# Optimization experiments

Hardware: AMD Instinct MI355X
Metric: run time of the kernel (lower is better)

## Reference

```python
import jax, jax.numpy as jnp
import numpy as np

N_NODES = 50000
N_EDGES = 200000
D = 384
R = 2  # num_relations


def setup_inputs() -> dict:
    key = jax.random.key(0)
    ks = jax.random.split(key, 16)
    inp = {
        "embeddings": jax.random.normal(ks[0], (N_NODES, D), dtype=jnp.float32),
        "edge_index": jax.random.randint(ks[1], (2, N_EDGES), 0, N_NODES, dtype=jnp.int64),
        "edge_type": jax.random.randint(ks[2], (N_EDGES,), 0, R, dtype=jnp.int64),
    }
    # RGCNConv params for 3 layers: per-relation weight, root weight, bias
    s = 1.0 / np.sqrt(D)
    for i, kk in zip((1, 2, 3), range(3)):
        inp[f"W{i}"] = jax.random.uniform(ks[3 + 3 * kk], (R, D, D), dtype=jnp.float32, minval=-s, maxval=s)
        inp[f"root{i}"] = jax.random.uniform(ks[4 + 3 * kk], (D, D), dtype=jnp.float32, minval=-s, maxval=s)
        inp[f"bias{i}"] = jnp.zeros((D,), dtype=jnp.float32)
    return inp


def _rgcn_conv(x, src, dst, edge_type, W, root, bias):
    # PyG RGCNConv with aggr='mean': for each relation, mean-aggregate neighbor
    # features over edges of that relation, then apply relation weight; plus
    # root transform and bias. We transform-then-aggregate (equivalent, linear).
    out = x @ root + bias
    for r in range(R):
        xr = x @ W[r]                                   # [N, D]
        mask = (edge_type == r).astype(x.dtype)         # [E]
        msg = xr[src] * mask[:, None]                   # [E, D] gather
        s = jax.ops.segment_sum(msg, dst, num_segments=N_NODES)    # [N, D]
        cnt = jax.ops.segment_sum(mask, dst, num_segments=N_NODES)  # [N]
        out = out + s / jnp.maximum(cnt, 1.0)[:, None]  # mean (0 if no edges)
    return out


def reference(embeddings, edge_index, edge_type, W1, root1, bias1, W2, root2, bias2, W3, root3, bias3):
    src, dst = edge_index[0], edge_index[1]
    x = jax.nn.relu(_rgcn_conv(embeddings, src, dst, edge_type, W1, root1, bias1))
    # dropout is identity in eval mode
    x = jax.nn.relu(_rgcn_conv(x, src, dst, edge_type, W2, root2, bias2))
    x = _rgcn_conv(x, src, dst, edge_type, W3, root3, bias3)
    return x
```

## Files before the change

### kernel.cpp

```cpp
#include <hip/hip_runtime.h>
#include <hip/hip_bf16.h>


#define D 384
#define NC 1152
#define BM 256
#define BN 192
#define BK 32
#define NKT (D / BK)
#define NTN (NC / BN)

typedef __attribute__((ext_vector_type(8))) short short8;
typedef __attribute__((ext_vector_type(4))) float floatx4;
typedef unsigned int uint;
typedef unsigned short ushort;

#define BAR() asm volatile("s_barrier" ::: "memory")
#define WAIT_LGKM0() asm volatile("s_waitcnt lgkmcnt(0)" ::: "memory")
#define WAIT_VM8() asm volatile("s_waitcnt vmcnt(8)" ::: "memory")
#define WAIT_VM4() asm volatile("s_waitcnt vmcnt(4)" ::: "memory")
#define WAIT_VM0() asm volatile("s_waitcnt vmcnt(0)" ::: "memory")

__device__ __forceinline__ void load_lds16(const void* g, void* l) {
    __builtin_amdgcn_global_load_lds(
        (const __attribute__((address_space(1))) void*)g,
        (__attribute__((address_space(3))) void*)l, 16, 0, 0);
}

__device__ __forceinline__ ushort f2bf(float x) {
    __hip_bfloat16 h = __float2bfloat16(x);
    return *reinterpret_cast<ushort*>(&h);
}

__device__ __forceinline__ uint pack2(float a, float b) {
    return (uint)f2bf(a) | ((uint)f2bf(b) << 16);
}

__device__ __forceinline__ void stage_tile(const ushort* __restrict__ g,
                                           ushort* l, int grow0, int kt,
                                           int rmax, int tid)
{
#pragma unroll
    for (int j = 0; j < 2; ++j) {
        const int ch = j * 512 + tid;
        const int row = ch >> 2;
        const int cs = ch & 3;
        const int gc = cs ^ ((row >> 1) & 3);
        const int gr = min(grow0 + row, rmax);
        load_lds16(g + (size_t)gr * D + kt * BK + gc * 8, l + (size_t)ch * 8);
    }
}

__global__ __launch_bounds__(512, 2) void gemm_bf16_mfma(
    const ushort* __restrict__ A, const ushort* __restrict__ BT,
    ushort* __restrict__ C, int M, int nwg)
{
    __shared__ alignas(16) ushort As[4][BM * BK];
    __shared__ alignas(16) ushort Bs[4][BM * BK];

    const int o = blockIdx.x;
    const int xcd = o & 7, lid = o >> 3;
    const int q = nwg >> 3, r = nwg & 7;
    const int wg = (xcd < r ? xcd * (q + 1) : r * (q + 1) + (xcd - r) * q) + lid;
    const int bnt = wg % NTN, bmt = wg / NTN;
    const int bm = bmt * BM, bn = bnt * BN;

    const int tid = threadIdx.x;
    const int wave = tid >> 6, lane = tid & 63;
    const int wn = wave >> 2;
    const int wm = wave & 3;
    const int l15 = lane & 15, k8 = lane >> 4;

    floatx4 acc[6][4] = {};

    stage_tile(A, As[0], bm, 0, M - 1, tid);
    stage_tile(BT, Bs[0], bn, 0, NC - 1, tid);
    stage_tile(A, As[1], bm, 1, M - 1, tid);
    stage_tile(BT, Bs[1], bn, 1, NC - 1, tid);
    stage_tile(A, As[2], bm, 2, M - 1, tid);
    stage_tile(BT, Bs[2], bn, 2, NC - 1, tid);
    WAIT_VM8();
    BAR();

    for (int j = 0; j < NKT; ++j) {
        const ushort* Ab = As[j & 3];
        const ushort* Bb = Bs[j & 3];

        short8 af[6], bf[4];
#pragma unroll
        for (int nf = 0; nf < 6; ++nf) {
            const int rr = wn * 96 + nf * 16 + l15;
            af[nf] = *(const short8*)(Bb + rr * BK + ((k8 ^ ((rr >> 1) & 3)) << 3));
        }
#pragma unroll
        for (int mf = 0; mf < 4; ++mf) {
            const int rr = wm * 64 + mf * 16 + l15;
            bf[mf] = *(const short8*)(Ab + rr * BK + ((k8 ^ ((rr >> 1) & 3)) << 3));
        }

        const int js = j + 3;
        if (js < NKT) {
            stage_tile(A, As[js & 3], bm, js, M - 1, tid);
            stage_tile(BT, Bs[js & 3], bn, js, NC - 1, tid);
        }

        WAIT_LGKM0();
        __builtin_amdgcn_sched_barrier(0);
        __builtin_amdgcn_s_setprio(1);
#pragma unroll
        for (int nf = 0; nf < 6; ++nf)
#pragma unroll
            for (int mf = 0; mf < 4; ++mf)
                acc[nf][mf] = __builtin_amdgcn_mfma_f32_16x16x32_bf16(
                    af[nf], bf[mf], acc[nf][mf], 0, 0, 0);
        __builtin_amdgcn_s_setprio(0);

        if (j <= NKT - 4)      { WAIT_VM8(); }
        else if (j == NKT - 3) { WAIT_VM4(); }
        else if (j == NKT - 2) { WAIT_VM0(); }
        BAR();
    }

    const int node0 = bm + wm * 64 + l15;
    const int col0 = bn + wn * 96 + k8 * 4;
    if (bm + BM <= M) {
#pragma unroll
        for (int mf = 0; mf < 4; ++mf) {
            uint2* rowp = (uint2*)(C + (size_t)(node0 + mf * 16) * NC + col0);
#pragma unroll
            for (int nf = 0; nf < 6; ++nf) {
                uint2 o2;
                o2.x = pack2(acc[nf][mf][0], acc[nf][mf][1]);
                o2.y = pack2(acc[nf][mf][2], acc[nf][mf][3]);
                rowp[nf * 4] = o2;
            }
        }
    } else {
#pragma unroll
        for (int mf = 0; mf < 4; ++mf) {
            const int node = node0 + mf * 16;
            if (node < M) {
                uint2* rowp = (uint2*)(C + (size_t)node * NC + col0);
#pragma unroll
                for (int nf = 0; nf < 6; ++nf) {
                    uint2 o2;
                    o2.x = pack2(acc[nf][mf][0], acc[nf][mf][1]);
                    o2.y = pack2(acc[nf][mf][2], acc[nf][mf][3]);
                    rowp[nf * 4] = o2;
                }
            }
        }
    }
}


__global__ __launch_bounds__(256) void count_edges(
    const int* __restrict__ dst, const int* __restrict__ et,
    int* __restrict__ cntI, int E, int M)
{
    const int e = blockIdx.x * blockDim.x + threadIdx.x;
    if (e < E) atomicAdd(&cntI[(size_t)et[e] * M + dst[e]], 1);
}

__global__ __launch_bounds__(256) void finalize_cnt(
    const int* __restrict__ cntI, float* __restrict__ invc, int n)
{
    const int i = blockIdx.x * blockDim.x + threadIdx.x;
    if (i < n) invc[i] = 1.0f / (float)max(cntI[i], 1);
}

__global__ __launch_bounds__(1024) void scan_local(
    const int* __restrict__ hist, int* __restrict__ offs,
    int* __restrict__ bsums, int n)
{
    __shared__ int tmp[1024];
    const int tid = threadIdx.x;
    const int i = blockIdx.x * 1024 + tid;
    const int v = (i < n) ? hist[i] : 0;
    tmp[tid] = v;
    __syncthreads();
#pragma unroll
    for (int off = 1; off < 1024; off <<= 1) {
        const int add = (tid >= off) ? tmp[tid - off] : 0;
        __syncthreads();
        tmp[tid] += add;
        __syncthreads();
    }
    if (i < n) offs[i] = tmp[tid] - v;
    if (tid == 1023) bsums[blockIdx.x] = tmp[1023];
}

__global__ __launch_bounds__(1024) void scan_bsums(
    int* __restrict__ bsums, int* __restrict__ total_out, int nb)
{
    __shared__ int tmp[1024];
    const int tid = threadIdx.x;
    const int v = (tid < nb) ? bsums[tid] : 0;
    tmp[tid] = v;
    __syncthreads();
#pragma unroll
    for (int off = 1; off < 1024; off <<= 1) {
        const int add = (tid >= off) ? tmp[tid - off] : 0;
        __syncthreads();
        tmp[tid] += add;
        __syncthreads();
    }
    if (tid < nb) bsums[tid] = tmp[tid] - v;
    if (tid == 1023) *total_out = tmp[1023];
}

__global__ __launch_bounds__(1024) void scan_add(
    int* __restrict__ offs, const int* __restrict__ bsums, int n)
{
    const int i = blockIdx.x * 1024 + threadIdx.x;
    if (i < n) offs[i] += bsums[blockIdx.x];
}

__global__ __launch_bounds__(256) void fill_sorted(
    const int* __restrict__ src, const int* __restrict__ dst,
    const int* __restrict__ et, const int* __restrict__ offs,
    int* __restrict__ cursor, int* __restrict__ sorted, int E, int M)
{
    const int e = blockIdx.x * blockDim.x + threadIdx.x;
    if (e < E) {
        const int key = et[e] * M + dst[e];
        const int pos = offs[key] + atomicAdd(&cursor[key], 1);
        sorted[pos] = src[e];
    }
}

__global__ __launch_bounds__(256) void build_bt(
    const float* __restrict__ root1, const float* __restrict__ W1,
    const float* __restrict__ root2, const float* __restrict__ W2,
    const float* __restrict__ root3, const float* __restrict__ W3,
    ushort* __restrict__ BT)
{
    __shared__ float tile[32][33];
    const int l = blockIdx.z;
    const float* root = (l == 0) ? root1 : (l == 1) ? root2 : root3;
    const float* W    = (l == 0) ? W1    : (l == 1) ? W2    : W3;
    const int kt = blockIdx.x * 32;
    const int nt = blockIdx.y * 32;
    const int tx = threadIdx.x & 31;
    const int ty = threadIdx.x >> 5;
    const float* srcm;
    int noff;
    if (nt < D)          { srcm = root;      noff = 0; }
    else if (nt < 2 * D) { srcm = W;         noff = D; }
    else                 { srcm = W + D * D; noff = 2 * D; }
    const int n = nt - noff + tx;
#pragma unroll
    for (int i = 0; i < 4; ++i) {
        const int k = kt + ty + i * 8;
        tile[ty + i * 8][tx] = srcm[(size_t)k * D + n];
    }
    __syncthreads();
    ushort* dst = BT + (size_t)l * NC * D;
#pragma unroll
    for (int i = 0; i < 4; ++i) {
        const int nn = nt + ty + i * 8;
        const int kk = kt + tx;
        dst[(size_t)nn * D + kk] = f2bf(tile[tx][ty + i * 8]);
    }
}

__global__ __launch_bounds__(256) void cast_f32_to_bf16(
    const float* __restrict__ x, ushort* __restrict__ y, int n4)
{
    const int i = blockIdx.x * blockDim.x + threadIdx.x;
    if (i < n4) {
        const float4 v = ((const float4*)x)[i];
        uint2 o;
        o.x = pack2(v.x, v.y);
        o.y = pack2(v.z, v.w);
        ((uint2*)y)[i] = o;
    }
}

__global__ __launch_bounds__(256) void aggregate_all(
    const ushort* __restrict__ TC, const int* __restrict__ sorted,
    const int* __restrict__ offs, const float* __restrict__ invc,
    const float* __restrict__ bias, ushort* __restrict__ outb,
    float* __restrict__ outf, int M, int relu)
{
    const int wave = threadIdx.x >> 6;
    const int lane = threadIdx.x & 63;
    const int d = blockIdx.x * 4 + wave;
    if (d >= M) return;

    float v[6];
    {
        const uint* rp = (const uint*)(TC + (size_t)d * NC);
#pragma unroll
        for (int p = 0; p < 3; ++p) {
            const uint b = rp[lane + 64 * p];
            const float2 bb = *(const float2*)(bias + (lane + 64 * p) * 2);
            v[2 * p]     = __uint_as_float(b << 16) + bb.x;
            v[2 * p + 1] = __uint_as_float(b & 0xffff0000u) + bb.y;
        }
    }
#pragma unroll
    for (int r = 0; r < 2; ++r) {
        const int key = r * M + d;
        const int beg = offs[key], end = offs[key + 1];
        float g[6] = {0.f, 0.f, 0.f, 0.f, 0.f, 0.f};
        for (int i = beg; i < end; ++i) {
            const int s = sorted[i];
            const uint* tp = (const uint*)(TC + (size_t)s * NC + D + r * D);
#pragma unroll
            for (int p = 0; p < 3; ++p) {
                const uint b = tp[lane + 64 * p];
                g[2 * p]     += __uint_as_float(b << 16);
                g[2 * p + 1] += __uint_as_float(b & 0xffff0000u);
            }
        }
        const float ic = invc[key];
#pragma unroll
        for (int j = 0; j < 6; ++j) v[j] += ic * g[j];
    }
    if (relu) {
#pragma unroll
        for (int j = 0; j < 6; ++j) v[j] = fmaxf(v[j], 0.f);
    }
    if (outb) {
        uint* op = (uint*)(outb + (size_t)d * D);
#pragma unroll
        for (int p = 0; p < 3; ++p) op[lane + 64 * p] = pack2(v[2 * p], v[2 * p + 1]);
    } else {
        float2* op = (float2*)(outf + (size_t)d * D);
#pragma unroll
        for (int p = 0; p < 3; ++p)
            op[lane + 64 * p] = make_float2(v[2 * p], v[2 * p + 1]);
    }
}

extern "C" void kernel_launch(void* const* d_in, const int* in_sizes, int n_in,
                              void* d_out, int out_size, void* d_ws, size_t ws_size,
                              hipStream_t stream)
{
    const float* emb   = (const float*)d_in[0];
    const int*   eidx  = (const int*)d_in[1];
    const int*   et    = (const int*)d_in[2];
    const float* W1    = (const float*)d_in[3];
    const float* root1 = (const float*)d_in[4];
    const float* bias1 = (const float*)d_in[5];
    const float* W2    = (const float*)d_in[6];
    const float* root2 = (const float*)d_in[7];
    const float* bias2 = (const float*)d_in[8];
    const float* W3    = (const float*)d_in[9];
    const float* root3 = (const float*)d_in[10];
    const float* bias3 = (const float*)d_in[11];

    float* out = (float*)d_out;
    const int M = in_sizes[0] / D;
    const int E = in_sizes[1] / 2;
    const int* src  = eidx;
    const int* dstv = eidx + E;

    const int n = 2 * M;
    const int nb = (n + 1023) / 1024;

    char* w = (char*)d_ws;
    ushort* TC = (ushort*)w;          w += (size_t)M * NC * 2;
    ushort* Xb = (ushort*)w;          w += (size_t)M * D * 2;
    ushort* BT = (ushort*)w;          w += (size_t)3 * NC * D * 2;
    float* invcnt = (float*)w;        w += (size_t)n * 4;
    int* cntI = (int*)w;              w += (size_t)n * 4;
    int* offs = (int*)w;              w += ((size_t)n + 1) * 4;
    int* sorted = (int*)w;            w += (size_t)E * 4;
    int* bsums = (int*)w;

    hipMemsetAsync(cntI, 0, (size_t)n * sizeof(int), stream);
    count_edges<<<(E + 255) / 256, 256, 0, stream>>>(dstv, et, cntI, E, M);
    finalize_cnt<<<(n + 255) / 256, 256, 0, stream>>>(cntI, invcnt, n);
    scan_local<<<nb, 1024, 0, stream>>>(cntI, offs, bsums, n);
    scan_bsums<<<1, 1024, 0, stream>>>(bsums, offs + n, nb);
    scan_add<<<nb, 1024, 0, stream>>>(offs, bsums, n);
    hipMemsetAsync(cntI, 0, (size_t)n * sizeof(int), stream);
    fill_sorted<<<(E + 255) / 256, 256, 0, stream>>>(src, dstv, et, offs, cntI, sorted, E, M);

    build_bt<<<dim3(D / 32, NC / 32, 3), 256, 0, stream>>>(root1, W1, root2, W2, root3, W3, BT);
    cast_f32_to_bf16<<<(M * D / 4 + 255) / 256, 256, 0, stream>>>(emb, Xb, M * D / 4);

    const int Mtiles = (M + BM - 1) / BM;
    const int nwg = Mtiles * NTN;
    const float* biases[3] = {bias1, bias2, bias3};
    for (int l = 0; l < 3; ++l) {
        gemm_bf16_mfma<<<nwg, 512, 0, stream>>>(Xb, BT + (size_t)l * NC * D, TC, M, nwg);
        const bool last = (l == 2);
        aggregate_all<<<(M + 3) / 4, 256, 0, stream>>>(
            TC, sorted, offs, invcnt, biases[l],
            last ? nullptr : Xb, last ? out : nullptr, M, last ? 0 : 1);
    }
}
```

Baseline: 548.5 us.

## Shrink GEMM N-tile to 128 with 3-stage LDS ring for higher occupancy

Reduces the GEMM tile from 256x192 to 256x128, switches the wave layout to 4x2, and cuts the LDS ring from four to three stages with a prefetch distance of two. Launch bounds rise to allow four workgroups per CU, aiming to hide latency through more resident waves and fewer registers per thread. It also drops the explicit LDS wait and sched_barrier before the MFMAs and leaves the compiler to place waits. In exchange each tile reuses less data, the grid gets more workgroups, and the shallower pipeline may expose memory latency.

```diff
diff --git a/kernel.cpp b/kernel.cpp
--- a/kernel.cpp
+++ b/kernel.cpp
@@ -5,7 +5,7 @@
 #define D 384
 #define NC 1152
 #define BM 256
-#define BN 192
+#define BN 128
 #define BK 32
 #define NKT (D / BK)
 #define NTN (NC / BN)
@@ -16,9 +16,7 @@
 typedef unsigned short ushort;
 
 #define BAR() asm volatile("s_barrier" ::: "memory")
-#define WAIT_LGKM0() asm volatile("s_waitcnt lgkmcnt(0)" ::: "memory")
-#define WAIT_VM8() asm volatile("s_waitcnt vmcnt(8)" ::: "memory")
-#define WAIT_VM4() asm volatile("s_waitcnt vmcnt(4)" ::: "memory")
+#define WAIT_VM3() asm volatile("s_waitcnt vmcnt(3)" ::: "memory")
 #define WAIT_VM0() asm volatile("s_waitcnt vmcnt(0)" ::: "memory")
 
 __device__ __forceinline__ void load_lds16(const void* g, void* l) {
@@ -36,9 +34,9 @@
     return (uint)f2bf(a) | ((uint)f2bf(b) << 16);
 }
 
-__device__ __forceinline__ void stage_tile(const ushort* __restrict__ g,
-                                           ushort* l, int grow0, int kt,
-                                           int rmax, int tid)
+__device__ __forceinline__ void stage_a(const ushort* __restrict__ g,
+                                        ushort* l, int grow0, int kt,
+                                        int rmax, int tid)
 {
 #pragma unroll
     for (int j = 0; j < 2; ++j) {
@@ -51,12 +49,22 @@
     }
 }
 
-__global__ __launch_bounds__(512, 2) void gemm_bf16_mfma(
+__device__ __forceinline__ void stage_b(const ushort* __restrict__ g,
+                                        ushort* l, int grow0, int kt, int tid)
+{
+    const int row = tid >> 2;
+    const int cs = tid & 3;
+    const int gc = cs ^ ((row >> 1) & 3);
+    load_lds16(g + (size_t)(grow0 + row) * D + kt * BK + gc * 8,
+               l + (size_t)tid * 8);
+}
+
+__global__ __launch_bounds__(512, 4) void gemm_bf16_mfma(
     const ushort* __restrict__ A, const ushort* __restrict__ BT,
     ushort* __restrict__ C, int M, int nwg)
 {
-    __shared__ alignas(16) ushort As[4][BM * BK];
-    __shared__ alignas(16) ushort Bs[4][BM * BK];
+    __shared__ alignas(16) ushort As[3][BM * BK];
+    __shared__ alignas(16) ushort Bs[3][BN * BK];
 
     const int o = blockIdx.x;
     const int xcd = o & 7, lid = o >> 3;
@@ -67,29 +75,27 @@
 
     const int tid = threadIdx.x;
     const int wave = tid >> 6, lane = tid & 63;
-    const int wn = wave >> 2;
-    const int wm = wave & 3;
+    const int wm = wave >> 1;
+    const int wn = wave & 1;
     const int l15 = lane & 15, k8 = lane >> 4;
 
-    floatx4 acc[6][4] = {};
-
-    stage_tile(A, As[0], bm, 0, M - 1, tid);
-    stage_tile(BT, Bs[0], bn, 0, NC - 1, tid);
-    stage_tile(A, As[1], bm, 1, M - 1, tid);
-    stage_tile(BT, Bs[1], bn, 1, NC - 1, tid);
-    stage_tile(A, As[2], bm, 2, M - 1, tid);
-    stage_tile(BT, Bs[2], bn, 2, NC - 1, tid);
-    WAIT_VM8();
+    floatx4 acc[4][4] = {};
+
+    stage_a(A, As[0], bm, 0, M - 1, tid);
+    stage_b(BT, Bs[0], bn, 0, tid);
+    stage_a(A, As[1], bm, 1, M - 1, tid);
+    stage_b(BT, Bs[1], bn, 1, tid);
+    WAIT_VM3();
     BAR();
 
     for (int j = 0; j < NKT; ++j) {
-        const ushort* Ab = As[j & 3];
-        const ushort* Bb = Bs[j & 3];
-
-        short8 af[6], bf[4];
-#pragma unroll
-        for (int nf = 0; nf < 6; ++nf) {
-            const int rr = wn * 96 + nf * 16 + l15;
+        const ushort* Ab = As[j % 3];
+        const ushort* Bb = Bs[j % 3];
+
+        short8 af[4], bf[4];
+#pragma unroll
+        for (int nf = 0; nf < 4; ++nf) {
+            const int rr = wn * 64 + nf * 16 + l15;
             af[nf] = *(const short8*)(Bb + rr * BK + ((k8 ^ ((rr >> 1) & 3)) << 3));
         }
 #pragma unroll
@@ -98,37 +104,34 @@
             bf[mf] = *(const short8*)(Ab + rr * BK + ((k8 ^ ((rr >> 1) & 3)) << 3));
         }
 
-        const int js = j + 3;
+        const int js = j + 2;
         if (js < NKT) {
-            stage_tile(A, As[js & 3], bm, js, M - 1, tid);
-            stage_tile(BT, Bs[js & 3], bn, js, NC - 1, tid);
-        }
-
-        WAIT_LGKM0();
-        __builtin_amdgcn_sched_barrier(0);
+            stage_a(A, As[js % 3], bm, js, M - 1, tid);
+            stage_b(BT, Bs[js % 3], bn, js, tid);
+        }
+
         __builtin_amdgcn_s_setprio(1);
 #pragma unroll
-        for (int nf = 0; nf < 6; ++nf)
+        for (int nf = 0; nf < 4; ++nf)
 #pragma unroll
             for (int mf = 0; mf < 4; ++mf)
                 acc[nf][mf] = __builtin_amdgcn_mfma_f32_16x16x32_bf16(
                     af[nf], bf[mf], acc[nf][mf], 0, 0, 0);
         __builtin_amdgcn_s_setprio(0);
 
-        if (j <= NKT - 4)      { WAIT_VM8(); }
-        else if (j == NKT - 3) { WAIT_VM4(); }
+        if (j <= NKT - 3)      { WAIT_VM3(); }
         else if (j == NKT - 2) { WAIT_VM0(); }
         BAR();
     }
 
     const int node0 = bm + wm * 64 + l15;
-    const int col0 = bn + wn * 96 + k8 * 4;
+    const int col0 = bn + wn * 64 + k8 * 4;
     if (bm + BM <= M) {
 #pragma unroll
         for (int mf = 0; mf < 4; ++mf) {
             uint2* rowp = (uint2*)(C + (size_t)(node0 + mf * 16) * NC + col0);
 #pragma unroll
-            for (int nf = 0; nf < 6; ++nf) {
+            for (int nf = 0; nf < 4; ++nf) {
                 uint2 o2;
                 o2.x = pack2(acc[nf][mf][0], acc[nf][mf][1]);
                 o2.y = pack2(acc[nf][mf][2], acc[nf][mf][3]);
@@ -142,7 +145,7 @@
             if (node < M) {
                 uint2* rowp = (uint2*)(C + (size_t)node * NC + col0);
 #pragma unroll
-                for (int nf = 0; nf < 6; ++nf) {
+                for (int nf = 0; nf < 4; ++nf) {
                     uint2 o2;
                     o2.x = pack2(acc[nf][mf][0], acc[nf][mf][1]);
                     o2.y = pack2(acc[nf][mf][2], acc[nf][mf][3]);
```

Result: faster. 510.5 us (-6.9%).
